# Performance work log

Measured on AMD Instinct MI355X. Metric: run time of the kernel, lower is better.

Reference implementation:

```python
import jax, jax.numpy as jnp
import numpy as np

B, T, D, H, E, TOPK = 2, 2048, 1024, 4096, 8, 2

def sq_relu(x):
    return jnp.square(jax.nn.relu(x))

def setup_inputs() -> dict:
    key = jax.random.key(0)
    ks = jax.random.split(key, 6)
    s = 0.02
    return {
        "x": jax.random.normal(ks[0], (B, T, D), dtype=jnp.float32),
        "W_router": jax.random.normal(ks[1], (D, E), dtype=jnp.float32) * s,   # [in, out]
        "W_up": jax.random.normal(ks[2], (E, D, H), dtype=jnp.float32) * s,
        "W_down": jax.random.normal(ks[3], (E, H, D), dtype=jnp.float32) * s,
        "W_sh_up": jax.random.normal(ks[4], (D, H), dtype=jnp.float32) * s,
        "W_sh_down": jax.random.normal(ks[5], (H, D), dtype=jnp.float32) * s,
    }

def reference(x, W_router, W_up, W_down, W_sh_up, W_sh_down):
    Bb, Tt, Dd = x.shape
    x_flat = x.reshape(-1, Dd)                                   # [N, D]
    N = x_flat.shape[0]
    logits = x_flat @ W_router                                   # [N, E]
    probs = jax.nn.sigmoid(logits)
    topk_probs, topk_idx = jax.lax.top_k(probs, TOPK)            # [N, k]
    topk_probs = topk_probs / (jnp.sum(topk_probs, axis=-1, keepdims=True) + 1e-6)
    # dense combine weights per (token, expert); equals routed prob or 0
    combine = jnp.zeros((N, E), dtype=x.dtype).at[
        jnp.arange(N)[:, None], topk_idx].add(topk_probs)        # [N, E]
    # shared expert
    out = sq_relu(x_flat @ W_sh_up) @ W_sh_down                  # [N, D]
    # routed experts: small fixed loop over E, weighted accumulate
    for e in range(E):
        h = sq_relu(x_flat @ W_up[e])                            # [N, H]
        out = out + combine[:, e:e + 1] * (h @ W_down[e])        # [N, D]
    return out.reshape(Bb, Tt, Dd)
```

## Files before the change

### kernel.cpp

```cpp
#include <hip/hip_runtime.h>

#define N_TOK 4096
#define DIM   1024
#define HID   4096
#define NSLOT 8192
#define TOTROWS 12288

typedef __bf16 bf16x8 __attribute__((ext_vector_type(8)));
typedef float  floatx4 __attribute__((ext_vector_type(4)));
typedef unsigned short us8 __attribute__((ext_vector_type(8)));
typedef unsigned short us4v __attribute__((ext_vector_type(4)));

static __device__ __forceinline__ unsigned short f2bf(float f) {
    unsigned u = __builtin_bit_cast(unsigned, f);
    unsigned r = 0x7fffu + ((u >> 16) & 1u);
    return (unsigned short)((u + r) >> 16);
}

__global__ void cvt_x_kernel(const float* __restrict__ x, unsigned short* __restrict__ xb) {
    int i = (blockIdx.x * 256 + threadIdx.x) * 4;
    float4 v = *(const float4*)(x + i);
    us4v o; o[0] = f2bf(v.x); o[1] = f2bf(v.y); o[2] = f2bf(v.z); o[3] = f2bf(v.w);
    *(us4v*)(xb + i) = o;
}

__global__ void router_kernel(const float* __restrict__ x, const float* __restrict__ Wr,
                              int* __restrict__ topk_idx, float* __restrict__ topk_w,
                              int* __restrict__ counts) {
    int lane = threadIdx.x & 63;
    int wave = threadIdx.x >> 6;
    int t = blockIdx.x * 4 + wave;
    const float* xr = x + (size_t)t * DIM;
    double acc[8];
    #pragma unroll
    for (int e = 0; e < 8; ++e) acc[e] = 0.0;
    #pragma unroll
    for (int it = 0; it < DIM / 64; ++it) {
        int d = it * 64 + lane;
        float xv = xr[d];
        const float* wr = Wr + (size_t)d * 8;
        float4 w0 = *(const float4*)wr;
        float4 w1 = *(const float4*)(wr + 4);
        acc[0] += (double)xv * w0.x; acc[1] += (double)xv * w0.y;
        acc[2] += (double)xv * w0.z; acc[3] += (double)xv * w0.w;
        acc[4] += (double)xv * w1.x; acc[5] += (double)xv * w1.y;
        acc[6] += (double)xv * w1.z; acc[7] += (double)xv * w1.w;
    }
    #pragma unroll
    for (int e = 0; e < 8; ++e) {
        #pragma unroll
        for (int off = 32; off > 0; off >>= 1)
            acc[e] += __shfl_xor(acc[e], off, 64);
    }
    if (lane == 0) {
        float p[8];
        #pragma unroll
        for (int e = 0; e < 8; ++e) p[e] = 1.0f / (1.0f + expf(-(float)acc[e]));
        int i0 = 0;
        for (int e = 1; e < 8; ++e) if (p[e] > p[i0]) i0 = e;
        int i1 = (i0 == 0) ? 1 : 0;
        for (int e = 0; e < 8; ++e) if (e != i0 && p[e] > p[i1]) i1 = e;
        float s = p[i0] + p[i1] + 1e-6f;
        topk_idx[t * 2]     = i0;
        topk_idx[t * 2 + 1] = i1;
        topk_w[t * 2]       = p[i0] / s;
        topk_w[t * 2 + 1]   = p[i1] / s;
        atomicAdd(&counts[i0], 1);
        atomicAdd(&counts[i1], 1);
    }
}

__global__ void scan_kernel(const int* __restrict__ counts, int* __restrict__ offsets) {
    if (threadIdx.x == 0) {
        int off = 0;
        for (int e = 0; e < 8; ++e) { offsets[e] = off; off += counts[e]; }
        offsets[8] = off;
    }
}

__global__ void assign_kernel(const int* __restrict__ topk_idx, const float* __restrict__ topk_w,
                              const int* __restrict__ offsets, int* __restrict__ cursors,
                              int* __restrict__ slot_token, float* __restrict__ slot_w,
                              int* __restrict__ token_slot) {
    int t = blockIdx.x * 256 + threadIdx.x;
    #pragma unroll
    for (int j = 0; j < 2; ++j) {
        int e = topk_idx[t * 2 + j];
        int pos = atomicAdd(&cursors[e], 1);
        int s = offsets[e] + pos;
        slot_token[s] = t;
        slot_w[s] = topk_w[t * 2 + j];
        token_slot[t * 2 + j] = s;
    }
    slot_token[NSLOT + t] = t;
    slot_w[NSLOT + t] = 1.0f;
}

template<int MODE>
__global__ void moe_gemm(const unsigned short* __restrict__ Abase,
                         const float* __restrict__ Wexp,
                         const float* __restrict__ Wsh,
                         unsigned short* __restrict__ Hout,
                         float* __restrict__ Yout,
                         const int* __restrict__ slot_token,
                         const float* __restrict__ slot_w,
                         const int* __restrict__ counts,
                         const int* __restrict__ offsets,
                         int K, int Nn, int lda)
{
    const int e   = blockIdx.z;
    const int cnt = (e == 8) ? N_TOK : counts[e];
    const int mt  = blockIdx.y;
    if (mt * 128 >= cnt) return;
    const int nt  = blockIdx.x;
    const int off = offsets[e];
    const float* Bp = (e == 8) ? Wsh : (Wexp + (size_t)e * K * Nn);

    __shared__ unsigned short As[128 * 40];
    __shared__ unsigned short Bs[128 * 40];

    const int t    = threadIdx.x;
    const int lane = t & 63;
    const int wave = t >> 6;
    const int wm   = wave >> 1, wn = wave & 1;
    const int m16  = lane & 15, quad = lane >> 4;
    const int kq   = quad * 8;

    const int arow0 = t >> 2;
    const int arow1 = 64 + (t >> 2);
    const int acol  = (t & 3) * 8;
    const unsigned short *ap0, *ap1;
    if (MODE == 0) {
        int tok0 = slot_token[off + mt * 128 + arow0];
        int tok1 = slot_token[off + mt * 128 + arow1];
        ap0 = Abase + (size_t)tok0 * lda + acol;
        ap1 = Abase + (size_t)tok1 * lda + acol;
    } else {
        ap0 = Abase + (size_t)(off + mt * 128 + arow0) * lda + acol;
        ap1 = Abase + (size_t)(off + mt * 128 + arow1) * lda + acol;
    }

    const int bn  = (t & 63) * 2;
    const int bkh = t >> 6;
    const float* bp = Bp + (size_t)(bkh * 8) * Nn + nt * 128 + bn;

    floatx4 acc[4][4];
    #pragma unroll
    for (int i = 0; i < 4; ++i)
        #pragma unroll
        for (int j = 0; j < 4; ++j)
            acc[i][j] = (floatx4){0.f, 0.f, 0.f, 0.f};

    const int nK = K / 32;
    for (int kt = 0; kt < nK; ++kt) {
        us8 a0 = *(const us8*)(ap0 + kt * 32);
        us8 a1 = *(const us8*)(ap1 + kt * 32);
        const float* bpk = bp + (size_t)kt * 32 * Nn;
        float2 bv[8];
        #pragma unroll
        for (int kk = 0; kk < 8; ++kk)
            bv[kk] = *(const float2*)(bpk + (size_t)kk * Nn);

        us8 c0, c1;
        #pragma unroll
        for (int kk = 0; kk < 8; ++kk) {
            c0[kk] = f2bf(bv[kk].x);
            c1[kk] = f2bf(bv[kk].y);
        }

        *(us8*)&As[arow0 * 40 + acol] = a0;
        *(us8*)&As[arow1 * 40 + acol] = a1;
        *(us8*)&Bs[bn * 40 + bkh * 8] = c0;
        *(us8*)&Bs[(bn + 1) * 40 + bkh * 8] = c1;
        __syncthreads();

        bf16x8 af[4], bfr[4];
        #pragma unroll
        for (int i = 0; i < 4; ++i)
            af[i] = *(const bf16x8*)&As[(wm * 64 + i * 16 + m16) * 40 + kq];
        #pragma unroll
        for (int j = 0; j < 4; ++j)
            bfr[j] = *(const bf16x8*)&Bs[(wn * 64 + j * 16 + m16) * 40 + kq];
        #pragma unroll
        for (int i = 0; i < 4; ++i)
            #pragma unroll
            for (int j = 0; j < 4; ++j)
                acc[i][j] = __builtin_amdgcn_mfma_f32_16x16x32_bf16(af[i], bfr[j], acc[i][j], 0, 0, 0);
        __syncthreads();
    }

    const int gn0 = nt * 128 + wn * 64 + m16;
    #pragma unroll
    for (int i = 0; i < 4; ++i) {
        const int lmb = mt * 128 + wm * 64 + i * 16 + quad * 4;
        #pragma unroll
        for (int r = 0; r < 4; ++r) {
            const int lm = lmb + r;
            if (lm < cnt) {
                size_t ro = (size_t)(off + lm) * Nn;
                if (MODE == 0) {
                    #pragma unroll
                    for (int j = 0; j < 4; ++j) {
                        float v = acc[i][j][r];
                        v = v > 0.f ? v * v : 0.f;
                        Hout[ro + gn0 + j * 16] = f2bf(v);
                    }
                } else {
                    float w = slot_w[off + lm];
                    #pragma unroll
                    for (int j = 0; j < 4; ++j)
                        Yout[ro + gn0 + j * 16] = w * acc[i][j][r];
                }
            }
        }
    }
}

__global__ void combine_kernel(const float* __restrict__ yg, const int* __restrict__ token_slot,
                               float* __restrict__ out) {
    int idx = blockIdx.x * 256 + threadIdx.x;
    int t = idx >> 8;
    int c = idx & 255;
    int s0 = token_slot[t * 2], s1 = token_slot[t * 2 + 1];
    const float4* y4 = (const float4*)yg;
    float4 a = y4[(size_t)s0 * 256 + c];
    float4 b = y4[(size_t)s1 * 256 + c];
    float4 d = y4[(size_t)(NSLOT + t) * 256 + c];
    float4 o;
    o.x = a.x + b.x + d.x;
    o.y = a.y + b.y + d.y;
    o.z = a.z + b.z + d.z;
    o.w = a.w + b.w + d.w;
    *((float4*)out + idx) = o;
}

extern "C" void kernel_launch(void* const* d_in, const int* in_sizes, int n_in,
                              void* d_out, int out_size, void* d_ws, size_t ws_size,
                              hipStream_t stream) {
    const float* x       = (const float*)d_in[0];
    const float* Wr      = (const float*)d_in[1];
    const float* Wup     = (const float*)d_in[2];
    const float* Wdown   = (const float*)d_in[3];
    const float* Wshup   = (const float*)d_in[4];
    const float* Wshdown = (const float*)d_in[5];
    float* out = (float*)d_out;

    char* ws = (char*)d_ws;
    unsigned short* xb = (unsigned short*)ws;
    unsigned short* hg = (unsigned short*)(ws + 8388608);
    float* yg          = (float*)(ws + 109051904);
    char* meta         = ws + 159383552;
    int*   counts      = (int*)meta;
    int*   cursors     = (int*)(meta + 64);
    int*   offsets     = (int*)(meta + 128);
    int*   topk_idx    = (int*)(meta + 256);
    float* topk_w      = (float*)(meta + 256 + 32768);
    int*   token_slot  = (int*)(meta + 256 + 65536);
    int*   slot_token  = (int*)(meta + 256 + 98304);
    float* slot_w      = (float*)(meta + 256 + 98304 + 49152);

    hipMemsetAsync(meta, 0, 128, stream);
    cvt_x_kernel<<<4096, 256, 0, stream>>>(x, xb);
    router_kernel<<<1024, 256, 0, stream>>>(x, Wr, topk_idx, topk_w, counts);
    scan_kernel<<<1, 64, 0, stream>>>(counts, offsets);
    assign_kernel<<<16, 256, 0, stream>>>(topk_idx, topk_w, offsets, cursors,
                                          slot_token, slot_w, token_slot);
    moe_gemm<0><<<dim3(32, 32, 9), 256, 0, stream>>>(xb, Wup, Wshup, hg, yg,
                                                     slot_token, slot_w, counts, offsets,
                                                     1024, 4096, 1024);
    moe_gemm<1><<<dim3(8, 32, 9), 256, 0, stream>>>(hg, Wdown, Wshdown, hg, yg,
                                                    slot_token, slot_w, counts, offsets,
                                                    4096, 1024, 4096);
    combine_kernel<<<4096, 256, 0, stream>>>(yg, token_slot, out);
}
```

Baseline: 903.6 us.

## Pre-transpose weights to bf16 and stage GEMM tiles with async global-to-LDS loads

Adds a transpose-and-convert pass that writes each weight matrix as bf16 in K-contiguous layout before each GEMM. The GEMM then fills both shared-memory tiles with direct 16-byte global_load_lds copies instead of strided fp32 loads followed by in-register conversion. The cost being removed is the uncoalesced fp32 weight reads and repeated conversion inside every tile that shares a weight column. In exchange it adds extra full passes over all weights and needs a larger workspace, keeping the old path as a fallback. The LDS padding is dropped, so fragment reads may now hit bank conflicts.

```diff
diff --git a/kernel.cpp b/kernel.cpp
--- a/kernel.cpp
+++ b/kernel.cpp
@@ -15,6 +15,13 @@
     unsigned u = __builtin_bit_cast(unsigned, f);
     unsigned r = 0x7fffu + ((u >> 16) & 1u);
     return (unsigned short)((u + r) >> 16);
+}
+
+static __device__ __forceinline__ void async16(const unsigned short* g, unsigned short* l) {
+    __builtin_amdgcn_global_load_lds(
+        (const __attribute__((address_space(1))) void*)g,
+        (__attribute__((address_space(3))) void*)l,
+        16, 0, 0);
 }
 
 __global__ void cvt_x_kernel(const float* __restrict__ x, unsigned short* __restrict__ xb) {
@@ -96,17 +103,45 @@
     slot_w[NSLOT + t] = 1.0f;
 }
 
+__global__ void transpose_cvt(const float* __restrict__ Wexp, const float* __restrict__ Wsh,
+                              unsigned short* __restrict__ outbuf, int R, int C) {
+    const int z = blockIdx.z;
+    const float* in = (z < 8) ? (Wexp + (size_t)z * R * C) : Wsh;
+    unsigned short* out = outbuf + (size_t)z * (size_t)R * C;
+    __shared__ float tile[64][65];
+    const int t   = threadIdx.x;
+    const int tr  = t >> 4;
+    const int tc4 = (t & 15) * 4;
+    const int gr0 = blockIdx.y * 64;
+    const int gc0 = blockIdx.x * 64;
+    #pragma unroll
+    for (int i = 0; i < 4; ++i) {
+        int r = i * 16 + tr;
+        float4 v = *(const float4*)(in + (size_t)(gr0 + r) * C + gc0 + tc4);
+        tile[r][tc4 + 0] = v.x; tile[r][tc4 + 1] = v.y;
+        tile[r][tc4 + 2] = v.z; tile[r][tc4 + 3] = v.w;
+    }
+    __syncthreads();
+    #pragma unroll
+    for (int i = 0; i < 4; ++i) {
+        int c = i * 16 + tr;
+        us4v o;
+        #pragma unroll
+        for (int j = 0; j < 4; ++j) o[j] = f2bf(tile[tc4 + j][c]);
+        *(us4v*)(out + (size_t)(gc0 + c) * R + gr0 + tc4) = o;
+    }
+}
+
 template<int MODE>
-__global__ void moe_gemm(const unsigned short* __restrict__ Abase,
-                         const float* __restrict__ Wexp,
-                         const float* __restrict__ Wsh,
-                         unsigned short* __restrict__ Hout,
-                         float* __restrict__ Yout,
-                         const int* __restrict__ slot_token,
-                         const float* __restrict__ slot_w,
-                         const int* __restrict__ counts,
-                         const int* __restrict__ offsets,
-                         int K, int Nn, int lda)
+__global__ void moe_gemm_a(const unsigned short* __restrict__ Abase,
+                           const unsigned short* __restrict__ Wt,
+                           unsigned short* __restrict__ Hout,
+                           float* __restrict__ Yout,
+                           const int* __restrict__ slot_token,
+                           const float* __restrict__ slot_w,
+                           const int* __restrict__ counts,
+                           const int* __restrict__ offsets,
+                           int K, int Nn, int lda)
 {
     const int e   = blockIdx.z;
     const int cnt = (e == 8) ? N_TOK : counts[e];
@@ -114,35 +149,35 @@
     if (mt * 128 >= cnt) return;
     const int nt  = blockIdx.x;
     const int off = offsets[e];
-    const float* Bp = (e == 8) ? Wsh : (Wexp + (size_t)e * K * Nn);
-
-    __shared__ unsigned short As[128 * 40];
-    __shared__ unsigned short Bs[128 * 40];
+
+    __shared__ unsigned short As[128 * 32];
+    __shared__ unsigned short Bs[128 * 32];
 
     const int t    = threadIdx.x;
     const int lane = t & 63;
     const int wave = t >> 6;
-    const int wm   = wave >> 1, wn = wave & 1;
-    const int m16  = lane & 15, quad = lane >> 4;
-    const int kq   = quad * 8;
-
-    const int arow0 = t >> 2;
-    const int arow1 = 64 + (t >> 2);
-    const int acol  = (t & 3) * 8;
-    const unsigned short *ap0, *ap1;
-    if (MODE == 0) {
-        int tok0 = slot_token[off + mt * 128 + arow0];
-        int tok1 = slot_token[off + mt * 128 + arow1];
-        ap0 = Abase + (size_t)tok0 * lda + acol;
-        ap1 = Abase + (size_t)tok1 * lda + acol;
-    } else {
-        ap0 = Abase + (size_t)(off + mt * 128 + arow0) * lda + acol;
-        ap1 = Abase + (size_t)(off + mt * 128 + arow1) * lda + acol;
-    }
-
-    const int bn  = (t & 63) * 2;
-    const int bkh = t >> 6;
-    const float* bp = Bp + (size_t)(bkh * 8) * Nn + nt * 128 + bn;
+
+    const unsigned short* agp[2];
+    const unsigned short* bgp[2];
+    unsigned short* aldst[2];
+    unsigned short* bldst[2];
+    #pragma unroll
+    for (int q = 0; q < 2; ++q) {
+        const int c   = wave * 2 + q;
+        const int row = c * 16 + (lane >> 2);
+        const int kc  = (lane & 3) * 8;
+        int arow;
+        if (MODE == 0) arow = slot_token[off + mt * 128 + row];
+        else           arow = off + mt * 128 + row;
+        agp[q]   = Abase + (size_t)arow * lda + kc;
+        bgp[q]   = Wt + (size_t)e * Nn * K + (size_t)(nt * 128 + row) * K + kc;
+        aldst[q] = &As[c * 512];
+        bldst[q] = &Bs[c * 512];
+    }
+
+    const int wm  = wave >> 1, wn = wave & 1;
+    const int m16 = lane & 15, quad = lane >> 4;
+    const int kq  = quad * 8;
 
     floatx4 acc[4][4];
     #pragma unroll
@@ -153,34 +188,21 @@
 
     const int nK = K / 32;
     for (int kt = 0; kt < nK; ++kt) {
-        us8 a0 = *(const us8*)(ap0 + kt * 32);
-        us8 a1 = *(const us8*)(ap1 + kt * 32);
-        const float* bpk = bp + (size_t)kt * 32 * Nn;
-        float2 bv[8];
-        #pragma unroll
-        for (int kk = 0; kk < 8; ++kk)
-            bv[kk] = *(const float2*)(bpk + (size_t)kk * Nn);
-
-        us8 c0, c1;
-        #pragma unroll
-        for (int kk = 0; kk < 8; ++kk) {
-            c0[kk] = f2bf(bv[kk].x);
-            c1[kk] = f2bf(bv[kk].y);
+        const int ko = kt * 32;
+        #pragma unroll
+        for (int q = 0; q < 2; ++q) {
+            async16(agp[q] + ko, aldst[q]);
+            async16(bgp[q] + ko, bldst[q]);
         }
-
-        *(us8*)&As[arow0 * 40 + acol] = a0;
-        *(us8*)&As[arow1 * 40 + acol] = a1;
-        *(us8*)&Bs[bn * 40 + bkh * 8] = c0;
-        *(us8*)&Bs[(bn + 1) * 40 + bkh * 8] = c1;
         __syncthreads();
 
         bf16x8 af[4], bfr[4];
         #pragma unroll
         for (int i = 0; i < 4; ++i)
-            af[i] = *(const bf16x8*)&As[(wm * 64 + i * 16 + m16) * 40 + kq];
+            af[i] = *(const bf16x8*)&As[(wm * 64 + i * 16 + m16) * 32 + kq];
         #pragma unroll
         for (int j = 0; j < 4; ++j)
-            bfr[j] = *(const bf16x8*)&Bs[(wn * 64 + j * 16 + m16) * 40 + kq];
+            bfr[j] = *(const bf16x8*)&Bs[(wn * 64 + j * 16 + m16) * 32 + kq];
         #pragma unroll
         for (int i = 0; i < 4; ++i)
             #pragma unroll
@@ -216,6 +238,126 @@
     }
 }
 
+template<int MODE>
+__global__ void moe_gemm_fb(const unsigned short* __restrict__ Abase,
+                            const float* __restrict__ Wexp,
+                            const float* __restrict__ Wsh,
+                            unsigned short* __restrict__ Hout,
+                            float* __restrict__ Yout,
+                            const int* __restrict__ slot_token,
+                            const float* __restrict__ slot_w,
+                            const int* __restrict__ counts,
+                            const int* __restrict__ offsets,
+                            int K, int Nn, int lda)
+{
+    const int e   = blockIdx.z;
+    const int cnt = (e == 8) ? N_TOK : counts[e];
+    const int mt  = blockIdx.y;
+    if (mt * 128 >= cnt) return;
+    const int nt  = blockIdx.x;
+    const int off = offsets[e];
+    const float* Bp = (e == 8) ? Wsh : (Wexp + (size_t)e * K * Nn);
+
+    __shared__ unsigned short As[128 * 40];
+    __shared__ unsigned short Bs[128 * 40];
+
+    const int t    = threadIdx.x;
+    const int lane = t & 63;
+    const int wave = t >> 6;
+    const int wm   = wave >> 1, wn = wave & 1;
+    const int m16  = lane & 15, quad = lane >> 4;
+    const int kq   = quad * 8;
+
+    const int arow0 = t >> 2;
+    const int arow1 = 64 + (t >> 2);
+    const int acol  = (t & 3) * 8;
+    const unsigned short *ap0, *ap1;
+    if (MODE == 0) {
+        int tok0 = slot_token[off + mt * 128 + arow0];
+        int tok1 = slot_token[off + mt * 128 + arow1];
+        ap0 = Abase + (size_t)tok0 * lda + acol;
+        ap1 = Abase + (size_t)tok1 * lda + acol;
+    } else {
+        ap0 = Abase + (size_t)(off + mt * 128 + arow0) * lda + acol;
+        ap1 = Abase + (size_t)(off + mt * 128 + arow1) * lda + acol;
+    }
+
+    const int bn  = (t & 63) * 2;
+    const int bkh = t >> 6;
+    const float* bp = Bp + (size_t)(bkh * 8) * Nn + nt * 128 + bn;
+
+    floatx4 acc[4][4];
+    #pragma unroll
+    for (int i = 0; i < 4; ++i)
+        #pragma unroll
+        for (int j = 0; j < 4; ++j)
+            acc[i][j] = (floatx4){0.f, 0.f, 0.f, 0.f};
+
+    const int nK = K / 32;
+    for (int kt = 0; kt < nK; ++kt) {
+        us8 a0 = *(const us8*)(ap0 + kt * 32);
+        us8 a1 = *(const us8*)(ap1 + kt * 32);
+        const float* bpk = bp + (size_t)kt * 32 * Nn;
+        float2 bv[8];
+        #pragma unroll
+        for (int kk = 0; kk < 8; ++kk)
+            bv[kk] = *(const float2*)(bpk + (size_t)kk * Nn);
+
+        us8 c0, c1;
+        #pragma unroll
+        for (int kk = 0; kk < 8; ++kk) {
+            c0[kk] = f2bf(bv[kk].x);
+            c1[kk] = f2bf(bv[kk].y);
+        }
+
+        *(us8*)&As[arow0 * 40 + acol] = a0;
+        *(us8*)&As[arow1 * 40 + acol] = a1;
+        *(us8*)&Bs[bn * 40 + bkh * 8] = c0;
+        *(us8*)&Bs[(bn + 1) * 40 + bkh * 8] = c1;
+        __syncthreads();
+
+        bf16x8 af[4], bfr[4];
+        #pragma unroll
+        for (int i = 0; i < 4; ++i)
+            af[i] = *(const bf16x8*)&As[(wm * 64 + i * 16 + m16) * 40 + kq];
+        #pragma unroll
+        for (int j = 0; j < 4; ++j)
+            bfr[j] = *(const bf16x8*)&Bs[(wn * 64 + j * 16 + m16) * 40 + kq];
+        #pragma unroll
+        for (int i = 0; i < 4; ++i)
+            #pragma unroll
+            for (int j = 0; j < 4; ++j)
+                acc[i][j] = __builtin_amdgcn_mfma_f32_16x16x32_bf16(af[i], bfr[j], acc[i][j], 0, 0, 0);
+        __syncthreads();
+    }
+
+    const int gn0 = nt * 128 + wn * 64 + m16;
+    #pragma unroll
+    for (int i = 0; i < 4; ++i) {
+        const int lmb = mt * 128 + wm * 64 + i * 16 + quad * 4;
+        #pragma unroll
+        for (int r = 0; r < 4; ++r) {
+            const int lm = lmb + r;
+            if (lm < cnt) {
+                size_t ro = (size_t)(off + lm) * Nn;
+                if (MODE == 0) {
+                    #pragma unroll
+                    for (int j = 0; j < 4; ++j) {
+                        float v = acc[i][j][r];
+                        v = v > 0.f ? v * v : 0.f;
+                        Hout[ro + gn0 + j * 16] = f2bf(v);
+                    }
+                } else {
+                    float w = slot_w[off + lm];
+                    #pragma unroll
+                    for (int j = 0; j < 4; ++j)
+                        Yout[ro + gn0 + j * 16] = w * acc[i][j][r];
+                }
+            }
+        }
+    }
+}
+
 __global__ void combine_kernel(const float* __restrict__ yg, const int* __restrict__ token_slot,
                                float* __restrict__ out) {
     int idx = blockIdx.x * 256 + threadIdx.x;
@@ -244,32 +386,66 @@
     const float* Wshup   = (const float*)d_in[4];
     const float* Wshdown = (const float*)d_in[5];
     float* out = (float*)d_out;
-
     char* ws = (char*)d_ws;
-    unsigned short* xb = (unsigned short*)ws;
-    unsigned short* hg = (unsigned short*)(ws + 8388608);
-    float* yg          = (float*)(ws + 109051904);
-    char* meta         = ws + 159383552;
-    int*   counts      = (int*)meta;
-    int*   cursors     = (int*)(meta + 64);
-    int*   offsets     = (int*)(meta + 128);
-    int*   topk_idx    = (int*)(meta + 256);
-    float* topk_w      = (float*)(meta + 256 + 32768);
-    int*   token_slot  = (int*)(meta + 256 + 65536);
-    int*   slot_token  = (int*)(meta + 256 + 98304);
-    float* slot_w      = (float*)(meta + 256 + 98304 + 49152);
-
-    hipMemsetAsync(meta, 0, 128, stream);
-    cvt_x_kernel<<<4096, 256, 0, stream>>>(x, xb);
-    router_kernel<<<1024, 256, 0, stream>>>(x, Wr, topk_idx, topk_w, counts);
-    scan_kernel<<<1, 64, 0, stream>>>(counts, offsets);
-    assign_kernel<<<16, 256, 0, stream>>>(topk_idx, topk_w, offsets, cursors,
-                                          slot_token, slot_w, token_slot);
-    moe_gemm<0><<<dim3(32, 32, 9), 256, 0, stream>>>(xb, Wup, Wshup, hg, yg,
-                                                     slot_token, slot_w, counts, offsets,
-                                                     1024, 4096, 1024);
-    moe_gemm<1><<<dim3(8, 32, 9), 256, 0, stream>>>(hg, Wdown, Wshdown, hg, yg,
-                                                    slot_token, slot_w, counts, offsets,
-                                                    4096, 1024, 4096);
-    combine_kernel<<<4096, 256, 0, stream>>>(yg, token_slot, out);
-}
+
+    const size_t NEEDED = 226492416ull + 262144ull;
+
+    if (ws_size >= NEEDED) {
+        unsigned short* hg = (unsigned short*)ws;
+        unsigned short* Wt = (unsigned short*)(ws + 100663296);
+        unsigned short* xb = (unsigned short*)(ws + 176160768);
+        float*          yg = (float*)(ws + 176160768);
+        char* meta         = ws + 226492416;
+        int*   counts      = (int*)meta;
+        int*   cursors     = (int*)(meta + 64);
+        int*   offsets     = (int*)(meta + 128);
+        int*   topk_idx    = (int*)(meta + 256);
+        float* topk_w      = (float*)(meta + 256 + 32768);
+        int*   token_slot  = (int*)(meta + 256 + 65536);
+        int*   slot_token  = (int*)(meta + 256 + 98304);
+        float* slot_w      = (float*)(meta + 256 + 98304 + 49152);
+
+        hipMemsetAsync(meta, 0, 128, stream);
+        cvt_x_kernel<<<4096, 256, 0, stream>>>(x, xb);
+        router_kernel<<<1024, 256, 0, stream>>>(x, Wr, topk_idx, topk_w, counts);
+        scan_kernel<<<1, 64, 0, stream>>>(counts, offsets);
+        assign_kernel<<<16, 256, 0, stream>>>(topk_idx, topk_w, offsets, cursors,
+                                              slot_token, slot_w, token_slot);
+        transpose_cvt<<<dim3(64, 16, 9), 256, 0, stream>>>(Wup, Wshup, Wt, 1024, 4096);
+        moe_gemm_a<0><<<dim3(32, 32, 9), 256, 0, stream>>>(xb, Wt, hg, yg,
+                                                           slot_token, slot_w, counts, offsets,
+                                                           1024, 4096, 1024);
+        transpose_cvt<<<dim3(16, 64, 9), 256, 0, stream>>>(Wdown, Wshdown, Wt, 4096, 1024);
+        moe_gemm_a<1><<<dim3(8, 32, 9), 256, 0, stream>>>(hg, Wt, hg, yg,
+                                                          slot_token, slot_w, counts, offsets,
+                                                          4096, 1024, 4096);
+        combine_kernel<<<4096, 256, 0, stream>>>(yg, token_slot, out);
+    } else {
+        unsigned short* xb = (unsigned short*)ws;
+        unsigned short* hg = (unsigned short*)(ws + 8388608);
+        float* yg          = (float*)(ws + 109051904);
+        char* meta         = ws + 159383552;
+        int*   counts      = (int*)meta;
+        int*   cursors     = (int*)(meta + 64);
+        int*   offsets     = (int*)(meta + 128);
+        int*   topk_idx    = (int*)(meta + 256);
+        float* topk_w      = (float*)(meta + 256 + 32768);
+        int*   token_slot  = (int*)(meta + 256 + 65536);
+        int*   slot_token  = (int*)(meta + 256 + 98304);
+        float* slot_w      = (float*)(meta + 256 + 98304 + 49152);
+
+        hipMemsetAsync(meta, 0, 128, stream);
+        cvt_x_kernel<<<4096, 256, 0, stream>>>(x, xb);
+        router_kernel<<<1024, 256, 0, stream>>>(x, Wr, topk_idx, topk_w, counts);
+        scan_kernel<<<1, 64, 0, stream>>>(counts, offsets);
+        assign_kernel<<<16, 256, 0, stream>>>(topk_idx, topk_w, offsets, cursors,
+                                              slot_token, slot_w, token_slot);
+        moe_gemm_fb<0><<<dim3(32, 32, 9), 256, 0, stream>>>(xb, Wup, Wshup, hg, yg,
+                                                            slot_token, slot_w, counts, offsets,
+                                                            1024, 4096, 1024);
+        moe_gemm_fb<1><<<dim3(8, 32, 9), 256, 0, stream>>>(hg, Wdown, Wshdown, hg, yg,
+                                                           slot_token, slot_w, counts, offsets,
+                                                           4096, 1024, 4096);
+        combine_kernel<<<4096, 256, 0, stream>>>(yg, token_slot, out);
+    }
+}
```

Measured after the change: 807.9 us. -10.6%, faster.
